# Performance work log

Hardware: AMD Instinct MI355X
Metric: run time of the kernel (lower is better)

## Reference

```python
import jax, jax.numpy as jnp
import numpy as np


def ste_sign(x):
    # larq ste_sign forward: sign(x) with sign(0) = 1
    return jnp.where(x >= 0, 1.0, -1.0).astype(x.dtype)


def setup_inputs() -> dict:
    key = jax.random.key(0)
    ks = jax.random.split(key, 8)
    B, H, W, Cin, Cout = 32, 56, 56, 256, 256
    x = jax.random.normal(ks[0], (B, H, W, Cin), dtype=jnp.float32)
    bias1 = jax.random.normal(ks[1], (1, 1, 1, Cin), dtype=jnp.float32) * 0.01
    kernel = jax.random.normal(ks[2], (3, 3, Cin, Cout), dtype=jnp.float32) * 0.1
    # BatchNormalization(scale=False): beta learnable, gamma=1, moving stats
    bn_beta = jax.random.normal(ks[3], (Cout,), dtype=jnp.float32) * 0.01
    bn_mean = jax.random.normal(ks[4], (Cout,), dtype=jnp.float32) * 0.01
    bn_var = jax.random.uniform(ks[5], (Cout,), dtype=jnp.float32, minval=0.5, maxval=1.5)
    bias2 = jax.random.normal(ks[6], (1, 1, 1, Cout), dtype=jnp.float32) * 0.01
    return {"x": x, "bias1": bias1, "kernel": kernel, "bn_beta": bn_beta,
            "bn_mean": bn_mean, "bn_var": bn_var, "bias2": bias2}


def reference(x, bias1, kernel, bn_beta, bn_mean, bn_var, bias2):
    eps = 1e-3  # keras BatchNormalization default epsilon
    strides = 1
    # lb_activation_1: learnable bias + ste_sign activation
    a = ste_sign(x + bias1)
    # QuantConv2D: binarize kernel, 'same' padding conv (NHWC, HWIO)
    qk = ste_sign(kernel)
    y = jax.lax.conv_general_dilated(
        a, qk, window_strides=(strides, strides), padding='SAME',
        dimension_numbers=('NHWC', 'HWIO', 'NHWC'))
    # BatchNormalization(scale=False) inference: (y - mean)/sqrt(var+eps) + beta
    y = (y - bn_mean) * jax.lax.rsqrt(bn_var + eps) + bn_beta
    # strides == 1: no avgpool residual branch
    # lb_activation_2: learnable bias + relu
    out = jax.nn.relu(y + bias2)
    return out
```

## Files before the change

### kernel.cpp

```cpp
#include <hip/hip_runtime.h>


typedef int v4i __attribute__((ext_vector_type(4)));
typedef unsigned int u32;

#define NB   32
#define HW   56
#define HP   58
#define HP2  (HP*HP)
#define CIN  256
#define COUT 256
#define NPIX (NB*HW*HW)
#define KTOT 2304
#define BM   128
#define NSTEP 36

#define PA_BYTES ((size_t)NB*HP*HP*CIN)
#define WT_OFF   PA_BYTES
#define WT_BYTES ((size_t)KTOT*COUT)
#define SC_OFF   (WT_OFF + WT_BYTES)
#define SH_OFF   (SC_OFF + 1024)

__device__ __forceinline__ void g2l16(const void* g, void* l) {
    __builtin_amdgcn_global_load_lds(
        (const __attribute__((address_space(1))) void*)g,
        (__attribute__((address_space(3))) void*)l, 16, 0, 0);
}

__global__ __launch_bounds__(256) void pack_a_kernel(
    const float* __restrict__ x, const float* __restrict__ b1,
    signed char* __restrict__ pa)
{
    const int lane = threadIdx.x & 63;
    const int pp = blockIdx.x * 4 + (threadIdx.x >> 6);
    const int n = pp / HP2, r = pp % HP2, ph = r / HP, pw = r % HP;
    const int ci = lane * 4;
    u32 o = 0;
    if (ph >= 1 && ph <= HW && pw >= 1 && pw <= HW) {
        const int pix = (n * HW + ph - 1) * HW + (pw - 1);
        const float4 xv = *(const float4*)(x + (size_t)pix * CIN + ci);
        const float4 bv = *(const float4*)(b1 + ci);
        o  = (u32)(unsigned char)((xv.x + bv.x >= 0.f) ? 1 : -1);
        o |= (u32)(unsigned char)((xv.y + bv.y >= 0.f) ? 1 : -1) << 8;
        o |= (u32)(unsigned char)((xv.z + bv.z >= 0.f) ? 1 : -1) << 16;
        o |= (u32)(unsigned char)((xv.w + bv.w >= 0.f) ? 1 : -1) << 24;
    }
    *(u32*)(pa + (size_t)pp * CIN + ci) = o;
}

__global__ __launch_bounds__(256) void packw_kernel(
    const float* __restrict__ k, signed char* __restrict__ wt)
{
    __shared__ signed char tile[64][256];
    const int t = threadIdx.x, k0 = blockIdx.x * 64;
    for (int j = 0; j < 64; ++j)
        tile[j][t] = (k[(size_t)(k0 + j) * COUT + t] >= 0.f) ? 1 : -1;
    __syncthreads();
    u32 wd[16];
#pragma unroll
    for (int j = 0; j < 16; ++j) wd[j] = 0;
#pragma unroll
    for (int j = 0; j < 64; ++j)
        wd[j >> 2] |= ((u32)(unsigned char)tile[j][t]) << ((j & 3) * 8);
    uint4* dst = (uint4*)(wt + (size_t)t * KTOT + k0);
#pragma unroll
    for (int j = 0; j < 4; ++j)
        dst[j] = make_uint4(wd[4*j], wd[4*j+1], wd[4*j+2], wd[4*j+3]);
}

__global__ __launch_bounds__(256) void bnprep_kernel(
    const float* __restrict__ beta, const float* __restrict__ mean,
    const float* __restrict__ var, const float* __restrict__ b2,
    float* __restrict__ scale, float* __restrict__ shift)
{
    const int t = threadIdx.x;
    const float s = rsqrtf(var[t] + 1e-3f);
    scale[t] = s;
    shift[t] = beta[t] - mean[t] * s + b2[t];
}

__global__ __launch_bounds__(256, 2) void conv_mfma_kernel(
    const signed char* __restrict__ pa, const signed char* __restrict__ wt,
    const float* __restrict__ scale, const float* __restrict__ shift,
    float* __restrict__ out)
{
    __shared__ signed char Al[2][BM * 64];
    __shared__ signed char Bl[2][COUT * 64];

    const int t = threadIdx.x, l = t & 63, v = t >> 6;
    const int p0 = blockIdx.x * BM;

    const signed char* abase[2];
#pragma unroll
    for (int i = 0; i < 2; ++i) {
        const int q = (t >> 2) + i * 64;
        const int p = p0 + q;
        const int n = p / 3136, r = p % 3136, h = r / 56, w = r % 56;
        const int aswz = (((t & 3) ^ ((q >> 1) & 3)) << 4);
        abase[i] = pa + ((size_t)(n * HP + h) * HP + w) * CIN + aswz;
    }

    const signed char* wbase[4];
#pragma unroll
    for (int j = 0; j < 4; ++j) {
        const int co = v * 64 + j * 16 + (l >> 2);
        const int bswz = (((l & 3) ^ ((co >> 1) & 3)) << 4);
        wbase[j] = wt + (size_t)co * KTOT + bswz;
    }

    int aoff[8], boff[4];
#pragma unroll
    for (int pg = 0; pg < 8; ++pg) {
        const int row = pg * 16 + (l & 15);
        aoff[pg] = row * 64 + ((((l >> 4) ^ (row >> 1)) & 3) << 4);
    }
#pragma unroll
    for (int cg = 0; cg < 4; ++cg) {
        const int row = v * 64 + cg * 16 + (l & 15);
        boff[cg] = row * 64 + ((((l >> 4) ^ (row >> 1)) & 3) << 4);
    }

    v4i acc[8][4];
#pragma unroll
    for (int i = 0; i < 8; ++i)
#pragma unroll
        for (int j = 0; j < 4; ++j) acc[i][j] = (v4i){0, 0, 0, 0};

    auto STAGE = [&](int buf, int s) {
        const int tap = s >> 2, cq = s & 3;
        const int ty = tap / 3, tx = tap - ty * 3;
        const int goff = ((ty * HP + tx) << 8) + (cq << 6);
        g2l16(abase[0] + goff, &Al[buf][v * 1024]);
        g2l16(abase[1] + goff, &Al[buf][4096 + v * 1024]);
#pragma unroll
        for (int j = 0; j < 4; ++j)
            g2l16(wbase[j] + (s << 6), &Bl[buf][v * 4096 + j * 1024]);
    };
    auto COMPUTE = [&](int cur) {
        v4i af[8], bf[4];
#pragma unroll
        for (int pg = 0; pg < 8; ++pg) af[pg] = *(const v4i*)(&Al[cur][aoff[pg]]);
#pragma unroll
        for (int cg = 0; cg < 4; ++cg) bf[cg] = *(const v4i*)(&Bl[cur][boff[cg]]);
#pragma unroll
        for (int pg = 0; pg < 8; ++pg)
#pragma unroll
            for (int cg = 0; cg < 4; ++cg)
                acc[pg][cg] = __builtin_amdgcn_mfma_i32_16x16x64_i8(
                    af[pg], bf[cg], acc[pg][cg], 0, 0, 0);
    };

    STAGE(0, 0);
    __syncthreads();
#pragma unroll 2
    for (int s = 0; s < NSTEP; ++s) {
        if (s + 1 < NSTEP) STAGE((s + 1) & 1, s + 1);
        COMPUTE(s & 1);
        __syncthreads();
    }

#pragma unroll
    for (int cg = 0; cg < 4; ++cg) {
        const int co = v * 64 + cg * 16 + (l & 15);
        const float sc = scale[co], sh = shift[co];
#pragma unroll
        for (int pg = 0; pg < 8; ++pg) {
            const int prow0 = p0 + pg * 16 + (l >> 4) * 4;
#pragma unroll
            for (int rr = 0; rr < 4; ++rr) {
                const float y = (float)acc[pg][cg][rr];
                out[(size_t)(prow0 + rr) * COUT + co] = fmaxf(fmaf(y, sc, sh), 0.f);
            }
        }
    }
}

extern "C" void kernel_launch(void* const* d_in, const int* in_sizes, int n_in,
                              void* d_out, int out_size, void* d_ws, size_t ws_size,
                              hipStream_t stream)
{
    const float* x      = (const float*)d_in[0];
    const float* bias1  = (const float*)d_in[1];
    const float* kernel = (const float*)d_in[2];
    const float* bn_beta = (const float*)d_in[3];
    const float* bn_mean = (const float*)d_in[4];
    const float* bn_var  = (const float*)d_in[5];
    const float* bias2   = (const float*)d_in[6];
    float* out = (float*)d_out;

    signed char* pa  = (signed char*)d_ws;
    signed char* wtp = (signed char*)d_ws + WT_OFF;
    float* scale = (float*)((char*)d_ws + SC_OFF);
    float* shift = (float*)((char*)d_ws + SH_OFF);

    pack_a_kernel<<<dim3(NB * HP2 / 4), dim3(256), 0, stream>>>(x, bias1, pa);
    packw_kernel<<<dim3(KTOT / 64), dim3(256), 0, stream>>>(kernel, wtp);
    bnprep_kernel<<<dim3(1), dim3(256), 0, stream>>>(bn_beta, bn_mean, bn_var, bias2,
                                                     scale, shift);
    conv_mfma_kernel<<<dim3(NPIX / BM), dim3(256), 0, stream>>>(pa, wtp, scale, shift, out);
}
```

Baseline: 114.4 us.

## Retile int8 conv GEMM to 128x128 tiles with 2x2 waves and grid swizzle

Changes the conv GEMM tile from 128 pixels x 256 channels to 128x128. Waves are arranged 2x2 so each wave holds 4x4 accumulators instead of 8x4, and the grid doubles with an XCD-style block swizzle. Each pipeline step now stages two 64-wide K slices, giving 18 steps. It also adds s_setprio around the MFMA burst and replaces __syncthreads with an explicit vmcnt wait plus barrier. The aim is higher occupancy and fewer barriers from the smaller register footprint, at the cost of loading A tiles twice across the channel halves.

```diff
diff --git a/kernel.cpp b/kernel.cpp
--- a/kernel.cpp
+++ b/kernel.cpp
@@ -13,7 +13,9 @@
 #define NPIX (NB*HW*HW)
 #define KTOT 2304
 #define BM   128
-#define NSTEP 36
+#define BN   128
+#define NSTEP 18
+#define NWG  ((NPIX/BM)*(COUT/BN))
 
 #define PA_BYTES ((size_t)NB*HP*HP*CIN)
 #define WT_OFF   PA_BYTES
@@ -84,11 +86,14 @@
     const float* __restrict__ scale, const float* __restrict__ shift,
     float* __restrict__ out)
 {
-    __shared__ signed char Al[2][BM * 64];
-    __shared__ signed char Bl[2][COUT * 64];
+    __shared__ signed char L[2][32768];
 
     const int t = threadIdx.x, l = t & 63, v = t >> 6;
-    const int p0 = blockIdx.x * BM;
+    const int vm = v >> 1, vn = v & 1;
+    const int swz  = (blockIdx.x & 7) * (NWG / 8) + (blockIdx.x >> 3);
+    const int tile = swz >> 1;
+    const int co0  = (swz & 1) << 7;
+    const int p0 = tile * BM;
 
     const signed char* abase[2];
 #pragma unroll
@@ -99,73 +104,89 @@
         const int aswz = (((t & 3) ^ ((q >> 1) & 3)) << 4);
         abase[i] = pa + ((size_t)(n * HP + h) * HP + w) * CIN + aswz;
     }
-
-    const signed char* wbase[4];
-#pragma unroll
-    for (int j = 0; j < 4; ++j) {
-        const int co = v * 64 + j * 16 + (l >> 2);
-        const int bswz = (((l & 3) ^ ((co >> 1) & 3)) << 4);
-        wbase[j] = wt + (size_t)co * KTOT + bswz;
-    }
-
-    int aoff[8], boff[4];
-#pragma unroll
-    for (int pg = 0; pg < 8; ++pg) {
-        const int row = pg * 16 + (l & 15);
+    const signed char* wbase[2];
+#pragma unroll
+    for (int j = 0; j < 2; ++j) {
+        const int r = j * 64 + (t >> 2);
+        const int bswz = (((t & 3) ^ ((r >> 1) & 3)) << 4);
+        wbase[j] = wt + (size_t)(co0 + r) * KTOT + bswz;
+    }
+
+    int aoff[4], boff[4];
+#pragma unroll
+    for (int pg = 0; pg < 4; ++pg) {
+        const int row = vm * 64 + pg * 16 + (l & 15);
         aoff[pg] = row * 64 + ((((l >> 4) ^ (row >> 1)) & 3) << 4);
     }
 #pragma unroll
     for (int cg = 0; cg < 4; ++cg) {
-        const int row = v * 64 + cg * 16 + (l & 15);
-        boff[cg] = row * 64 + ((((l >> 4) ^ (row >> 1)) & 3) << 4);
-    }
-
-    v4i acc[8][4];
-#pragma unroll
-    for (int i = 0; i < 8; ++i)
+        const int row = vn * 64 + cg * 16 + (l & 15);
+        boff[cg] = 16384 + row * 64 + ((((l >> 4) ^ (row >> 1)) & 3) << 4);
+    }
+
+    v4i acc[4][4];
+#pragma unroll
+    for (int i = 0; i < 4; ++i)
 #pragma unroll
         for (int j = 0; j < 4; ++j) acc[i][j] = (v4i){0, 0, 0, 0};
 
+    auto goffA = [&](int k64) {
+        const int tap = k64 >> 2, cq = k64 & 3;
+        const int ty = tap / 3, tx = tap - ty * 3;
+        return ((ty * HP + tx) << 8) + (cq << 6);
+    };
     auto STAGE = [&](int buf, int s) {
-        const int tap = s >> 2, cq = s & 3;
-        const int ty = tap / 3, tx = tap - ty * 3;
-        const int goff = ((ty * HP + tx) << 8) + (cq << 6);
-        g2l16(abase[0] + goff, &Al[buf][v * 1024]);
-        g2l16(abase[1] + goff, &Al[buf][4096 + v * 1024]);
-#pragma unroll
-        for (int j = 0; j < 4; ++j)
-            g2l16(wbase[j] + (s << 6), &Bl[buf][v * 4096 + j * 1024]);
+#pragma unroll
+        for (int ks = 0; ks < 2; ++ks) {
+            const int k64 = 2 * s + ks;
+            const int go = goffA(k64);
+            g2l16(abase[0] + go, &L[buf][ks * 8192 + v * 1024]);
+            g2l16(abase[1] + go, &L[buf][ks * 8192 + 4096 + v * 1024]);
+            g2l16(wbase[0] + (k64 << 6), &L[buf][16384 + ks * 8192 + v * 1024]);
+            g2l16(wbase[1] + (k64 << 6), &L[buf][16384 + ks * 8192 + 4096 + v * 1024]);
+        }
     };
-    auto COMPUTE = [&](int cur) {
-        v4i af[8], bf[4];
-#pragma unroll
-        for (int pg = 0; pg < 8; ++pg) af[pg] = *(const v4i*)(&Al[cur][aoff[pg]]);
-#pragma unroll
-        for (int cg = 0; cg < 4; ++cg) bf[cg] = *(const v4i*)(&Bl[cur][boff[cg]]);
-#pragma unroll
-        for (int pg = 0; pg < 8; ++pg)
+
+    STAGE(0, 0);
+    asm volatile("s_waitcnt vmcnt(0)" ::: "memory");
+    __builtin_amdgcn_s_barrier();
+
+#pragma unroll 1
+    for (int s = 0; s < NSTEP; ++s) {
+        const int cur = s & 1, nxt = cur ^ 1;
+        const signed char* Lc = &L[cur][0];
+        if (s + 1 < NSTEP) STAGE(nxt, s + 1);
+        v4i af[2][4], bf[2][4];
+#pragma unroll
+        for (int ks = 0; ks < 2; ++ks) {
+#pragma unroll
+            for (int pg = 0; pg < 4; ++pg)
+                af[ks][pg] = *(const v4i*)(Lc + ks * 8192 + aoff[pg]);
 #pragma unroll
             for (int cg = 0; cg < 4; ++cg)
-                acc[pg][cg] = __builtin_amdgcn_mfma_i32_16x16x64_i8(
-                    af[pg], bf[cg], acc[pg][cg], 0, 0, 0);
-    };
-
-    STAGE(0, 0);
-    __syncthreads();
-#pragma unroll 2
-    for (int s = 0; s < NSTEP; ++s) {
-        if (s + 1 < NSTEP) STAGE((s + 1) & 1, s + 1);
-        COMPUTE(s & 1);
-        __syncthreads();
+                bf[ks][cg] = *(const v4i*)(Lc + ks * 8192 + boff[cg]);
+        }
+        __builtin_amdgcn_s_setprio(1);
+#pragma unroll
+        for (int ks = 0; ks < 2; ++ks)
+#pragma unroll
+            for (int pg = 0; pg < 4; ++pg)
+#pragma unroll
+                for (int cg = 0; cg < 4; ++cg)
+                    acc[pg][cg] = __builtin_amdgcn_mfma_i32_16x16x64_i8(
+                        af[ks][pg], bf[ks][cg], acc[pg][cg], 0, 0, 0);
+        __builtin_amdgcn_s_setprio(0);
+        asm volatile("s_waitcnt vmcnt(0)" ::: "memory");
+        __builtin_amdgcn_s_barrier();
     }
 
 #pragma unroll
     for (int cg = 0; cg < 4; ++cg) {
-        const int co = v * 64 + cg * 16 + (l & 15);
+        const int co = co0 + vn * 64 + cg * 16 + (l & 15);
         const float sc = scale[co], sh = shift[co];
 #pragma unroll
-        for (int pg = 0; pg < 8; ++pg) {
-            const int prow0 = p0 + pg * 16 + (l >> 4) * 4;
+        for (int pg = 0; pg < 4; ++pg) {
+            const int prow0 = p0 + vm * 64 + pg * 16 + (l >> 4) * 4;
 #pragma unroll
             for (int rr = 0; rr < 4; ++rr) {
                 const float y = (float)acc[pg][cg][rr];
@@ -197,5 +218,5 @@
     packw_kernel<<<dim3(KTOT / 64), dim3(256), 0, stream>>>(kernel, wtp);
     bnprep_kernel<<<dim3(1), dim3(256), 0, stream>>>(bn_beta, bn_mean, bn_var, bias2,
                                                      scale, shift);
-    conv_mfma_kernel<<<dim3(NPIX / BM), dim3(256), 0, stream>>>(pa, wtp, scale, shift, out);
-}
+    conv_mfma_kernel<<<dim3(NWG), dim3(256), 0, stream>>>(pa, wtp, scale, shift, out);
+}
```

New measurement: 102.9 us (median of 2 runs). 1.11x faster.

## Rework conv main loop sync, LDS layout, and block order for XCD locality

Applied to the files above, without the earlier changes.

Merges the A and B shared buffers into one array and changes the weight staging mapping so each wave loads a contiguous 1KB slice. The main loop is rewritten to wait on vmcnt and issue a raw barrier rather than __syncthreads, with unroll 1 and s_setprio around the MFMA block. Block indices are remapped in groups of eight so neighbouring pixel tiles land on the same XCD for L2 reuse. These aim to cut synchronisation and stall overhead, at the cost of relying on manual waitcnt correctness.

```diff
diff --git a/kernel.cpp b/kernel.cpp
--- a/kernel.cpp
+++ b/kernel.cpp
@@ -13,7 +13,9 @@
 #define NPIX (NB*HW*HW)
 #define KTOT 2304
 #define BM   128
+#define BN   256
 #define NSTEP 36
+#define NWG  (NPIX/BM)
 
 #define PA_BYTES ((size_t)NB*HP*HP*CIN)
 #define WT_OFF   PA_BYTES
@@ -84,11 +86,11 @@
     const float* __restrict__ scale, const float* __restrict__ shift,
     float* __restrict__ out)
 {
-    __shared__ signed char Al[2][BM * 64];
-    __shared__ signed char Bl[2][COUT * 64];
+    __shared__ signed char L[2][24576];
 
     const int t = threadIdx.x, l = t & 63, v = t >> 6;
-    const int p0 = blockIdx.x * BM;
+    const int swz = (blockIdx.x & 7) * (NWG / 8) + (blockIdx.x >> 3);
+    const int p0 = swz * BM;
 
     const signed char* abase[2];
 #pragma unroll
@@ -99,13 +101,12 @@
         const int aswz = (((t & 3) ^ ((q >> 1) & 3)) << 4);
         abase[i] = pa + ((size_t)(n * HP + h) * HP + w) * CIN + aswz;
     }
-
     const signed char* wbase[4];
 #pragma unroll
     for (int j = 0; j < 4; ++j) {
-        const int co = v * 64 + j * 16 + (l >> 2);
-        const int bswz = (((l & 3) ^ ((co >> 1) & 3)) << 4);
-        wbase[j] = wt + (size_t)co * KTOT + bswz;
+        const int r = j * 64 + (t >> 2);
+        const int bswz = (((t & 3) ^ ((r >> 1) & 3)) << 4);
+        wbase[j] = wt + (size_t)r * KTOT + bswz;
     }
 
     int aoff[8], boff[4];
@@ -117,7 +118,7 @@
 #pragma unroll
     for (int cg = 0; cg < 4; ++cg) {
         const int row = v * 64 + cg * 16 + (l & 15);
-        boff[cg] = row * 64 + ((((l >> 4) ^ (row >> 1)) & 3) << 4);
+        boff[cg] = 8192 + row * 64 + ((((l >> 4) ^ (row >> 1)) & 3) << 4);
     }
 
     v4i acc[8][4];
@@ -126,37 +127,47 @@
 #pragma unroll
         for (int j = 0; j < 4; ++j) acc[i][j] = (v4i){0, 0, 0, 0};
 
-    auto STAGE = [&](int buf, int s) {
+    auto goffA = [&](int s) {
         const int tap = s >> 2, cq = s & 3;
         const int ty = tap / 3, tx = tap - ty * 3;
-        const int goff = ((ty * HP + tx) << 8) + (cq << 6);
-        g2l16(abase[0] + goff, &Al[buf][v * 1024]);
-        g2l16(abase[1] + goff, &Al[buf][4096 + v * 1024]);
+        return ((ty * HP + tx) << 8) + (cq << 6);
+    };
+    auto STAGE = [&](int buf, int s) {
+        const int go = goffA(s);
+        g2l16(abase[0] + go, &L[buf][v * 1024]);
+        g2l16(abase[1] + go, &L[buf][4096 + v * 1024]);
 #pragma unroll
         for (int j = 0; j < 4; ++j)
-            g2l16(wbase[j] + (s << 6), &Bl[buf][v * 4096 + j * 1024]);
+            g2l16(wbase[j] + (s << 6), &L[buf][8192 + j * 4096 + v * 1024]);
     };
-    auto COMPUTE = [&](int cur) {
-        v4i af[8], bf[4];
-#pragma unroll
-        for (int pg = 0; pg < 8; ++pg) af[pg] = *(const v4i*)(&Al[cur][aoff[pg]]);
-#pragma unroll
-        for (int cg = 0; cg < 4; ++cg) bf[cg] = *(const v4i*)(&Bl[cur][boff[cg]]);
-#pragma unroll
-        for (int pg = 0; pg < 8; ++pg)
-#pragma unroll
-            for (int cg = 0; cg < 4; ++cg)
-                acc[pg][cg] = __builtin_amdgcn_mfma_i32_16x16x64_i8(
-                    af[pg], bf[cg], acc[pg][cg], 0, 0, 0);
-    };
 
     STAGE(0, 0);
-    __syncthreads();
-#pragma unroll 2
+    asm volatile("s_waitcnt vmcnt(0)" ::: "memory");
+    __builtin_amdgcn_s_barrier();
+
+#pragma unroll 1
     for (int s = 0; s < NSTEP; ++s) {
-        if (s + 1 < NSTEP) STAGE((s + 1) & 1, s + 1);
-        COMPUTE(s & 1);
-        __syncthreads();
+        const int cur = s & 1, nxt = cur ^ 1;
+        const signed char* Lc = &L[cur][0];
+        if (s + 1 < NSTEP) STAGE(nxt, s + 1);
+        v4i bf0 = *(const v4i*)(Lc + boff[0]);
+        v4i bf1 = *(const v4i*)(Lc + boff[1]);
+        v4i bf2 = *(const v4i*)(Lc + boff[2]);
+        v4i bf3 = *(const v4i*)(Lc + boff[3]);
+        v4i af[8];
+#pragma unroll
+        for (int pg = 0; pg < 8; ++pg) af[pg] = *(const v4i*)(Lc + aoff[pg]);
+        __builtin_amdgcn_s_setprio(1);
+#pragma unroll
+        for (int pg = 0; pg < 8; ++pg) {
+            acc[pg][0] = __builtin_amdgcn_mfma_i32_16x16x64_i8(af[pg], bf0, acc[pg][0], 0, 0, 0);
+            acc[pg][1] = __builtin_amdgcn_mfma_i32_16x16x64_i8(af[pg], bf1, acc[pg][1], 0, 0, 0);
+            acc[pg][2] = __builtin_amdgcn_mfma_i32_16x16x64_i8(af[pg], bf2, acc[pg][2], 0, 0, 0);
+            acc[pg][3] = __builtin_amdgcn_mfma_i32_16x16x64_i8(af[pg], bf3, acc[pg][3], 0, 0, 0);
+        }
+        __builtin_amdgcn_s_setprio(0);
+        asm volatile("s_waitcnt vmcnt(0)" ::: "memory");
+        __builtin_amdgcn_s_barrier();
     }
 
 #pragma unroll
@@ -197,5 +208,5 @@
     packw_kernel<<<dim3(KTOT / 64), dim3(256), 0, stream>>>(kernel, wtp);
     bnprep_kernel<<<dim3(1), dim3(256), 0, stream>>>(bn_beta, bn_mean, bn_var, bias2,
                                                      scale, shift);
-    conv_mfma_kernel<<<dim3(NPIX / BM), dim3(256), 0, stream>>>(pa, wtp, scale, shift, out);
-}
+    conv_mfma_kernel<<<dim3(NWG), dim3(256), 0, stream>>>(pa, wtp, scale, shift, out);
+}
```

Result: faster. 104.4 us (-8.7%).

## Load MFMA operands directly from global into registers, dropping LDS staging

Applied to the files above, without the earlier changes.

The conv kernel no longer stages A and B tiles through LDS with global_load_lds and barriers. Each wave now loads its own fragments straight from global memory into registers, double-buffered across two steps. It also remaps the block index so consecutive workgroups are spread across pixel ranges. This removes the LDS round trip and the __syncthreads. In exchange, each of the four waves fetches the same A rows redundantly from global/L2, and register pressure rises with the two fragment buffers.

```diff
diff --git a/kernel.cpp b/kernel.cpp
--- a/kernel.cpp
+++ b/kernel.cpp
@@ -14,18 +14,13 @@
 #define KTOT 2304
 #define BM   128
 #define NSTEP 36
+#define NWG  (NPIX/BM)
 
 #define PA_BYTES ((size_t)NB*HP*HP*CIN)
 #define WT_OFF   PA_BYTES
 #define WT_BYTES ((size_t)KTOT*COUT)
 #define SC_OFF   (WT_OFF + WT_BYTES)
 #define SH_OFF   (SC_OFF + 1024)
-
-__device__ __forceinline__ void g2l16(const void* g, void* l) {
-    __builtin_amdgcn_global_load_lds(
-        (const __attribute__((address_space(1))) void*)g,
-        (__attribute__((address_space(3))) void*)l, 16, 0, 0);
-}
 
 __global__ __launch_bounds__(256) void pack_a_kernel(
     const float* __restrict__ x, const float* __restrict__ b1,
@@ -79,45 +74,49 @@
     shift[t] = beta[t] - mean[t] * s + b2[t];
 }
 
+
+#define LOAD_TILE(AF, BF, S)                                                  \
+    {                                                                         \
+        const int tap_ = (S) >> 2, cq_ = (S) & 3;                             \
+        const u32 gA_ = (u32)((((tap_ / 3) * HP + (tap_ % 3)) << 8) + (cq_ << 6)); \
+        const u32 gB_ = (u32)((S) << 6);                                      \
+        _Pragma("unroll")                                                     \
+        for (int pg = 0; pg < 8; ++pg)                                        \
+            AF[pg] = *(const v4i*)(pa + aB[pg] + gA_);                        \
+        _Pragma("unroll")                                                     \
+        for (int cg = 0; cg < 4; ++cg)                                        \
+            BF[cg] = *(const v4i*)(wt + bB[cg] + gB_);                        \
+    }
+
+#define MFMA_TILE(AF, BF)                                                     \
+    _Pragma("unroll")                                                         \
+    for (int pg = 0; pg < 8; ++pg) {                                          \
+        _Pragma("unroll")                                                     \
+        for (int cg = 0; cg < 4; ++cg)                                        \
+            acc[pg][cg] = __builtin_amdgcn_mfma_i32_16x16x64_i8(              \
+                AF[pg], BF[cg], acc[pg][cg], 0, 0, 0);                        \
+    }
+
 __global__ __launch_bounds__(256, 2) void conv_mfma_kernel(
     const signed char* __restrict__ pa, const signed char* __restrict__ wt,
     const float* __restrict__ scale, const float* __restrict__ shift,
     float* __restrict__ out)
 {
-    __shared__ signed char Al[2][BM * 64];
-    __shared__ signed char Bl[2][COUT * 64];
+    const int t = threadIdx.x, l = t & 63, w = t >> 6;
+    const int swz = (blockIdx.x & 7) * (NWG / 8) + (blockIdx.x >> 3);
+    const int p0 = swz * BM;
 
-    const int t = threadIdx.x, l = t & 63, v = t >> 6;
-    const int p0 = blockIdx.x * BM;
-
-    const signed char* abase[2];
-#pragma unroll
-    for (int i = 0; i < 2; ++i) {
-        const int q = (t >> 2) + i * 64;
-        const int p = p0 + q;
-        const int n = p / 3136, r = p % 3136, h = r / 56, w = r % 56;
-        const int aswz = (((t & 3) ^ ((q >> 1) & 3)) << 4);
-        abase[i] = pa + ((size_t)(n * HP + h) * HP + w) * CIN + aswz;
-    }
-
-    const signed char* wbase[4];
-#pragma unroll
-    for (int j = 0; j < 4; ++j) {
-        const int co = v * 64 + j * 16 + (l >> 2);
-        const int bswz = (((l & 3) ^ ((co >> 1) & 3)) << 4);
-        wbase[j] = wt + (size_t)co * KTOT + bswz;
-    }
-
-    int aoff[8], boff[4];
+    u32 aB[8], bB[4];
 #pragma unroll
     for (int pg = 0; pg < 8; ++pg) {
-        const int row = pg * 16 + (l & 15);
-        aoff[pg] = row * 64 + ((((l >> 4) ^ (row >> 1)) & 3) << 4);
+        const int p = p0 + pg * 16 + (l & 15);
+        const int n = p / 3136, r = p % 3136, h = r / 56, ww = r % 56;
+        aB[pg] = (u32)(((n * HP + h) * HP + ww) * CIN + ((l >> 4) << 4));
     }
 #pragma unroll
     for (int cg = 0; cg < 4; ++cg) {
-        const int row = v * 64 + cg * 16 + (l & 15);
-        boff[cg] = row * 64 + ((((l >> 4) ^ (row >> 1)) & 3) << 4);
+        const int co = w * 64 + cg * 16 + (l & 15);
+        bB[cg] = (u32)(co * KTOT + ((l >> 4) << 4));
     }
 
     v4i acc[8][4];
@@ -126,42 +125,20 @@
 #pragma unroll
         for (int j = 0; j < 4; ++j) acc[i][j] = (v4i){0, 0, 0, 0};
 
-    auto STAGE = [&](int buf, int s) {
-        const int tap = s >> 2, cq = s & 3;
-        const int ty = tap / 3, tx = tap - ty * 3;
-        const int goff = ((ty * HP + tx) << 8) + (cq << 6);
-        g2l16(abase[0] + goff, &Al[buf][v * 1024]);
-        g2l16(abase[1] + goff, &Al[buf][4096 + v * 1024]);
-#pragma unroll
-        for (int j = 0; j < 4; ++j)
-            g2l16(wbase[j] + (s << 6), &Bl[buf][v * 4096 + j * 1024]);
-    };
-    auto COMPUTE = [&](int cur) {
-        v4i af[8], bf[4];
-#pragma unroll
-        for (int pg = 0; pg < 8; ++pg) af[pg] = *(const v4i*)(&Al[cur][aoff[pg]]);
-#pragma unroll
-        for (int cg = 0; cg < 4; ++cg) bf[cg] = *(const v4i*)(&Bl[cur][boff[cg]]);
-#pragma unroll
-        for (int pg = 0; pg < 8; ++pg)
-#pragma unroll
-            for (int cg = 0; cg < 4; ++cg)
-                acc[pg][cg] = __builtin_amdgcn_mfma_i32_16x16x64_i8(
-                    af[pg], bf[cg], acc[pg][cg], 0, 0, 0);
-    };
+    v4i aX[8], bX[4], aY[8], bY[4];
 
-    STAGE(0, 0);
-    __syncthreads();
-#pragma unroll 2
-    for (int s = 0; s < NSTEP; ++s) {
-        if (s + 1 < NSTEP) STAGE((s + 1) & 1, s + 1);
-        COMPUTE(s & 1);
-        __syncthreads();
+    LOAD_TILE(aX, bX, 0)
+#pragma unroll 1
+    for (int s = 0; s < NSTEP; s += 2) {
+        LOAD_TILE(aY, bY, s + 1)
+        MFMA_TILE(aX, bX)
+        if (s + 2 < NSTEP) LOAD_TILE(aX, bX, s + 2)
+        MFMA_TILE(aY, bY)
     }
 
 #pragma unroll
     for (int cg = 0; cg < 4; ++cg) {
-        const int co = v * 64 + cg * 16 + (l & 15);
+        const int co = w * 64 + cg * 16 + (l & 15);
         const float sc = scale[co], sh = shift[co];
 #pragma unroll
         for (int pg = 0; pg < 8; ++pg) {
@@ -197,5 +174,5 @@
     packw_kernel<<<dim3(KTOT / 64), dim3(256), 0, stream>>>(kernel, wtp);
     bnprep_kernel<<<dim3(1), dim3(256), 0, stream>>>(bn_beta, bn_mean, bn_var, bias2,
                                                      scale, shift);
-    conv_mfma_kernel<<<dim3(NPIX / BM), dim3(256), 0, stream>>>(pa, wtp, scale, shift, out);
+    conv_mfma_kernel<<<dim3(NWG), dim3(256), 0, stream>>>(pa, wtp, scale, shift, out);
 }
```

New measurement: 226.9 us. 1.98x slower.
